# Optimization experiments

Hardware: AMD Instinct MI355X
Metric: run time of the kernel (lower is better)

## Reference

```python
import jax, jax.numpy as jnp
import numpy as np

N_NODES = 100000
N_EDGES = 1600000
IN_DIM = 128
HID = 32
HEADS = 4
NEG_SLOPE = 0.2


def gat_conv(x, src, dst, W, att_src, att_dst, bias, n_nodes, heads, out_ch):
    # x: [N, Fin], W: [Fin, heads*out_ch], att_*: [heads, out_ch], bias: [heads*out_ch]
    h = (x @ W).reshape(n_nodes, heads, out_ch)            # [N, H, C]
    a_src = jnp.einsum('nhc,hc->nh', h, att_src)           # [N, H]
    a_dst = jnp.einsum('nhc,hc->nh', h, att_dst)           # [N, H]
    e = jax.nn.leaky_relu(a_src[src] + a_dst[dst], NEG_SLOPE)  # [E, H]
    # segment softmax over incoming edges of each target node
    e_max = jax.ops.segment_max(e, dst, num_segments=n_nodes)  # [N, H]
    ex = jnp.exp(e - e_max[dst])                               # [E, H]
    denom = jax.ops.segment_sum(ex, dst, num_segments=n_nodes)  # [N, H]
    alpha = ex / denom[dst]                                     # [E, H]
    msg = h[src] * alpha[:, :, None]                            # [E, H, C]
    out = jax.ops.segment_sum(msg, dst, num_segments=n_nodes)   # [N, H, C]
    return out.reshape(n_nodes, heads * out_ch) + bias


def setup_inputs() -> dict:
    key = jax.random.key(0)
    ks = jax.random.split(key, 10)
    x = jax.random.normal(ks[0], (N_NODES, IN_DIM), dtype=jnp.float32)
    edge_index = jax.random.randint(ks[1], (2, N_EDGES), 0, N_NODES, dtype=jnp.int64) if jax.config.jax_enable_x64 else jax.random.randint(ks[1], (2, N_EDGES), 0, N_NODES, dtype=jnp.int32)
    s = 0.1
    W1 = jax.random.normal(ks[2], (IN_DIM, HEADS * HID), dtype=jnp.float32) * s
    att_src1 = jax.random.normal(ks[3], (HEADS, HID), dtype=jnp.float32) * s
    att_dst1 = jax.random.normal(ks[4], (HEADS, HID), dtype=jnp.float32) * s
    b1 = jnp.zeros((HEADS * HID,), dtype=jnp.float32)
    W2 = jax.random.normal(ks[5], (HEADS * HID, HEADS * HID), dtype=jnp.float32) * s
    att_src2 = jax.random.normal(ks[6], (HEADS, HID), dtype=jnp.float32) * s
    att_dst2 = jax.random.normal(ks[7], (HEADS, HID), dtype=jnp.float32) * s
    b2 = jnp.zeros((HEADS * HID,), dtype=jnp.float32)
    return {"x": x, "edge_index": edge_index, "W1": W1, "att_src1": att_src1,
            "att_dst1": att_dst1, "b1": b1, "W2": W2, "att_src2": att_src2,
            "att_dst2": att_dst2, "b2": b2}


def reference(x, edge_index, W1, att_src1, att_dst1, b1, W2, att_src2, att_dst2, b2):
    src, dst = edge_index[0], edge_index[1]
    x1 = jax.nn.relu(gat_conv(x, src, dst, W1, att_src1, att_dst1, b1, N_NODES, HEADS, HID))
    x2 = jax.nn.relu(gat_conv(x1, src, dst, W2, att_src2, att_dst2, b2, N_NODES, HEADS, HID))
    # [N, heads*hid, 2]
    return jnp.concatenate([x1[:, :, None], x2[:, :, None]], axis=2)
```

## Files before the change

kernel.cpp:

```cpp
#include <hip/hip_runtime.h>

#define NN 100000
#define NE 1600000
#define GEMM_GRID 1563
#define NBUK 196
#define BCAP 10240
#define PA_BLOCKS 320
#define PA_EDGES 5000
#define K1_GRID (16 + PA_BLOCKS)
#define K2_GRID (NBUK + GEMM_GRID)
#define AGG_GRID 12500

typedef short bf16x8 __attribute__((ext_vector_type(8)));
typedef float f32x4 __attribute__((ext_vector_type(4)));
typedef unsigned int u32;
typedef u32 u32x4 __attribute__((ext_vector_type(4)));
typedef unsigned short u16;

__device__ inline u32 bf16r(float x) {
    u32 u = __float_as_uint(x);
    return (u + 0x7FFFu + ((u >> 16) & 1u)) >> 16;
}

__device__ inline void split_pack8(const float a[8], u32 hh[4], u32 ll[4]) {
#pragma unroll
    for (int j = 0; j < 4; ++j) {
        u32 u0 = __float_as_uint(a[2 * j]);
        u32 u1 = __float_as_uint(a[2 * j + 1]);
        float l0 = a[2 * j] - __uint_as_float(u0 & 0xFFFF0000u);
        float l1 = a[2 * j + 1] - __uint_as_float(u1 & 0xFFFF0000u);
        hh[j] = (u0 >> 16) | (u1 & 0xFFFF0000u);
        ll[j] = (__float_as_uint(l0) >> 16) | (__float_as_uint(l1) & 0xFFFF0000u);
    }
}

__device__ inline void wpack_body(int idx, const float* __restrict__ W,
                                  bf16x8* __restrict__ wpH, bf16x8* __restrict__ wpL) {
    if (idx >= 2048) return;
    int lane = idx & 63, tile = idx >> 6;
    int kc = tile >> 3, ct = tile & 7;
    int col = lane & 15, kq = lane >> 4;
    int kbase = kc * 32 + kq * 8;
    float a[8];
#pragma unroll
    for (int i = 0; i < 8; ++i)
        a[i] = W[(size_t)(kbase + i) * 128 + ct * 16 + col];
    u32 hh[4], ll[4];
    split_pack8(a, hh, ll);
    wpH[tile * 64 + lane] = __builtin_bit_cast(bf16x8, (u32x4){hh[0], hh[1], hh[2], hh[3]});
    wpL[tile * 64 + lane] = __builtin_bit_cast(bf16x8, (u32x4){ll[0], ll[1], ll[2], ll[3]});
}

__global__ __launch_bounds__(256) void k1(
    const float* __restrict__ W1, bf16x8* __restrict__ wpH1, bf16x8* __restrict__ wpL1,
    const float* __restrict__ W2, bf16x8* __restrict__ wpH2, bf16x8* __restrict__ wpL2,
    const int* __restrict__ dst, const int* __restrict__ src,
    int* __restrict__ gtail, u32* __restrict__ tmp) {
    const int b = blockIdx.x;
    if (b < 8) {
        wpack_body(b * 256 + threadIdx.x, W1, wpH1, wpL1);
        return;
    } else if (b < 16) {
        wpack_body((b - 8) * 256 + threadIdx.x, W2, wpH2, wpL2);
        return;
    }
    __shared__ int lhist[NBUK], lcur[NBUK];
    const int t = threadIdx.x;
    const int e0 = (b - 16) * PA_EDGES;
    const int e1 = e0 + PA_EDGES;
    for (int i = t; i < NBUK; i += 256) lhist[i] = 0;
    __syncthreads();
    for (int e = e0 + t; e < e1; e += 256)
        atomicAdd(&lhist[dst[e] >> 9], 1);
    __syncthreads();
    for (int i = t; i < NBUK; i += 256)
        if (lhist[i] > 0) lcur[i] = atomicAdd(&gtail[i], lhist[i]);
    __syncthreads();
    for (int e = e0 + t; e < e1; e += 256) {
        int d = dst[e];
        int bb = d >> 9;
        int p = atomicAdd(&lcur[bb], 1);
        tmp[(size_t)bb * BCAP + p] = ((u32)(d & 511) << 17) | (u32)src[e];
    }
}

__device__ inline void gemm_epilogue(f32x4 acc[8], int row0, int w, int col, int kq,
                                     const float* __restrict__ atts,
                                     const float* __restrict__ attd,
                                     u16* __restrict__ hb,
                                     float* __restrict__ a_src,
                                     float* __restrict__ a_dst) {
    float as0[4], as1[4], ad0[4], ad1[4];
#pragma unroll
    for (int q = 0; q < 4; ++q) {
        as0[q] = atts[q * 32 + col];
        as1[q] = atts[q * 32 + 16 + col];
        ad0[q] = attd[q * 32 + col];
        ad1[q] = attd[q * 32 + 16 + col];
    }
#pragma unroll
    for (int r = 0; r < 4; ++r) {
        int node = row0 + w * 16 + kq * 4 + r;
        float ps[4], pd[4];
#pragma unroll
        for (int q = 0; q < 4; ++q) {
            float d0 = acc[2 * q][r], d1 = acc[2 * q + 1][r];
            ps[q] = d0 * as0[q] + d1 * as1[q];
            pd[q] = d0 * ad0[q] + d1 * ad1[q];
        }
#pragma unroll
        for (int off = 1; off < 16; off <<= 1) {
#pragma unroll
            for (int q = 0; q < 4; ++q) {
                ps[q] += __shfl_xor(ps[q], off);
                pd[q] += __shfl_xor(pd[q], off);
            }
        }
        if (node < NN) {
#pragma unroll
            for (int ct = 0; ct < 8; ++ct)
                hb[(size_t)node * 128 + ct * 16 + col] = (u16)bf16r(acc[ct][r]);
            if (col < 4) {
                float vs = col == 0 ? ps[0] : col == 1 ? ps[1] : col == 2 ? ps[2] : ps[3];
                float vd = col == 0 ? pd[0] : col == 1 ? pd[1] : col == 2 ? pd[2] : pd[3];
                a_src[node * 4 + col] = vs;
                a_dst[node * 4 + col] = vd;
            }
        }
    }
}

__global__ __launch_bounds__(256) void k2(
    const float* __restrict__ x,
    const bf16x8* __restrict__ wpH, const bf16x8* __restrict__ wpL,
    const float* __restrict__ atts, const float* __restrict__ attd,
    u16* __restrict__ hb, float* __restrict__ a_src, float* __restrict__ a_dst,
    const int* __restrict__ gtail, const u32* __restrict__ tmp,
    int* __restrict__ row_ptr, int* __restrict__ src_sorted) {
    __shared__ u32 ldata[BCAP];
    __shared__ int lh[512];
    __shared__ int lsc[256];
    __shared__ int wsum[4];
    const int idx = blockIdx.x;
    const int t = threadIdx.x;
    if (idx < NBUK) {
        const int g = idx;
        const int n = gtail[g];
        int gv = (t < g) ? gtail[t] : 0;
#pragma unroll
        for (int m = 1; m < 64; m <<= 1) gv += __shfl_xor(gv, m);
        if ((t & 63) == 0) wsum[t >> 6] = gv;
        lh[t] = 0;
        lh[t + 256] = 0;
        __syncthreads();
        const int ebase = wsum[0] + wsum[1] + wsum[2] + wsum[3];
        for (int i = t; i < n; i += 256) ldata[i] = tmp[(size_t)g * BCAP + i];
        __syncthreads();
        for (int i = t; i < n; i += 256)
            atomicAdd(&lh[ldata[i] >> 17], 1);
        __syncthreads();
        int c0 = lh[2 * t], c1 = lh[2 * t + 1];
        lsc[t] = c0 + c1;
        __syncthreads();
        for (int off = 1; off < 256; off <<= 1) {
            int xv = (t >= off) ? lsc[t - off] : 0;
            __syncthreads();
            lsc[t] += xv;
            __syncthreads();
        }
        int exclPair = (t == 0) ? 0 : lsc[t - 1];
        int base0 = ebase + exclPair;
        int base1 = base0 + c0;
        lh[2 * t] = base0;
        lh[2 * t + 1] = base1;
        int node = (g << 9) + 2 * t;
        if (node < NN) row_ptr[node] = base0;
        if (node + 1 < NN) row_ptr[node + 1] = base1;
        if (g == NBUK - 1 && t == 0) row_ptr[NN] = ebase + n;
        __syncthreads();
        for (int i = t; i < n; i += 256) {
            u32 v = ldata[i];
            int p = atomicAdd(&lh[v >> 17], 1);
            src_sorted[p] = (int)(v & 0x1FFFFu);
        }
        return;
    }
    const int row0 = (idx - NBUK) * 64;
    const int lane = t & 63;
    const int w = t >> 6;
    const int col = lane & 15, kq = lane >> 4;
    int node_a = row0 + w * 16 + col;
    if (node_a > NN - 1) node_a = NN - 1;
    const float* xrow = x + (size_t)node_a * 128 + kq * 8;
    float a[32];
#pragma unroll
    for (int kc = 0; kc < 4; ++kc) {
        *(float4*)&a[kc * 8 + 0] = *(const float4*)(xrow + kc * 32);
        *(float4*)&a[kc * 8 + 4] = *(const float4*)(xrow + kc * 32 + 4);
    }
    f32x4 acc[8];
#pragma unroll
    for (int ct = 0; ct < 8; ++ct) acc[ct] = (f32x4){0.f, 0.f, 0.f, 0.f};
#pragma unroll
    for (int kc = 0; kc < 4; ++kc) {
        u32 hh[4], ll[4];
        split_pack8(&a[kc * 8], hh, ll);
        bf16x8 ah = __builtin_bit_cast(bf16x8, (u32x4){hh[0], hh[1], hh[2], hh[3]});
        bf16x8 al = __builtin_bit_cast(bf16x8, (u32x4){ll[0], ll[1], ll[2], ll[3]});
#pragma unroll
        for (int ct = 0; ct < 8; ++ct) {
            bf16x8 bh = wpH[(kc * 8 + ct) * 64 + lane];
            bf16x8 bl = wpL[(kc * 8 + ct) * 64 + lane];
            acc[ct] = __builtin_amdgcn_mfma_f32_16x16x32_bf16(ah, bh, acc[ct], 0, 0, 0);
            acc[ct] = __builtin_amdgcn_mfma_f32_16x16x32_bf16(al, bh, acc[ct], 0, 0, 0);
            acc[ct] = __builtin_amdgcn_mfma_f32_16x16x32_bf16(ah, bl, acc[ct], 0, 0, 0);
        }
    }
    gemm_epilogue(acc, row0, w, col, kq, atts, attd, hb, a_src, a_dst);
}

__global__ __launch_bounds__(256) void k_gemm2(
    const u32* __restrict__ xb,
    const bf16x8* __restrict__ wpH, const bf16x8* __restrict__ wpL,
    const float* __restrict__ atts, const float* __restrict__ attd,
    u16* __restrict__ hb, float* __restrict__ a_src, float* __restrict__ a_dst) {
    const int t = threadIdx.x;
    const int row0 = blockIdx.x * 64;
    const int lane = t & 63;
    const int w = t >> 6;
    const int col = lane & 15, kq = lane >> 4;
    int node_a = row0 + w * 16 + col;
    if (node_a > NN - 1) node_a = NN - 1;
    const u32* xrow = xb + (size_t)node_a * 64 + kq * 4;
    int4 aw[4];
#pragma unroll
    for (int kc = 0; kc < 4; ++kc) aw[kc] = *(const int4*)(xrow + kc * 16);
    f32x4 acc[8];
#pragma unroll
    for (int ct = 0; ct < 8; ++ct) acc[ct] = (f32x4){0.f, 0.f, 0.f, 0.f};
#pragma unroll
    for (int kc = 0; kc < 4; ++kc) {
        bf16x8 a = __builtin_bit_cast(bf16x8, aw[kc]);
#pragma unroll
        for (int ct = 0; ct < 8; ++ct) {
            bf16x8 bh = wpH[(kc * 8 + ct) * 64 + lane];
            bf16x8 bl = wpL[(kc * 8 + ct) * 64 + lane];
            acc[ct] = __builtin_amdgcn_mfma_f32_16x16x32_bf16(a, bh, acc[ct], 0, 0, 0);
            acc[ct] = __builtin_amdgcn_mfma_f32_16x16x32_bf16(a, bl, acc[ct], 0, 0, 0);
        }
    }
    gemm_epilogue(acc, row0, w, col, kq, atts, attd, hb, a_src, a_dst);
}

__global__ __launch_bounds__(256, 4) void k_agg(
    const u32* __restrict__ hb,
    const float* __restrict__ a_src, const float* __restrict__ a_dst,
    const int* __restrict__ row_ptr, const int* __restrict__ src_sorted,
    const float* __restrict__ bias,
    u32* __restrict__ x1b, float* __restrict__ outp, int layer) {
    const int lane = threadIdx.x & 63;
    const int node0 = blockIdx.x * 8 + (threadIdx.x >> 6) * 2;
    const int q = lane >> 4;
    const int es = lane & 15;
    const int hbase = lane & 48;
#pragma unroll
    for (int ni = 0; ni < 2; ++ni) {
        const int node = node0 + ni;
        if (node >= NN) continue;
        const int e0 = row_ptr[node], e1 = row_ptr[node + 1];
        const int emax = e1 - 1;
        const float advh = a_dst[node * 4 + q];
        float den = 0.f, a0a = 0.f, a0b = 0.f, a1a = 0.f, a1b = 0.f;
        if (e1 > e0) {
            int eidx = e0 + es;
            if (eidx > emax) eidx = emax;
            int sv = src_sorted[eidx];
            float av = a_src[sv * 4 + q];
            for (int ec = e0; ec < e1; ec += 16) {
                int cnt = e1 - ec;
                cnt = cnt < 16 ? cnt : 16;
                int eidxn = ec + 16 + es;
                if (eidxn > emax) eidxn = emax;
                int svn = src_sorted[eidxn];
                float avn = a_src[svn * 4 + q];
                float lk = av + advh;
                lk = lk > 0.f ? lk : 0.2f * lk;
                float ex = (es < cnt) ? __expf(lk - 8.f) : 0.f;
                den += ex;
                if (cnt == 16) {
                    u32 wv[16];
#pragma unroll
                    for (int u = 0; u < 16; ++u) {
                        int su = __builtin_amdgcn_readlane(sv, u);
                        wv[u] = hb[((size_t)su << 6) + lane];
                    }
                    float exu[16];
#pragma unroll
                    for (int u = 0; u < 16; ++u) exu[u] = __shfl(ex, hbase | u);
#pragma unroll
                    for (int u = 0; u < 16; ++u) {
                        float h0 = __uint_as_float(wv[u] << 16);
                        float h1 = __uint_as_float(wv[u] & 0xFFFF0000u);
                        if (u & 1) { a0b = fmaf(exu[u], h0, a0b); a1b = fmaf(exu[u], h1, a1b); }
                        else       { a0a = fmaf(exu[u], h0, a0a); a1a = fmaf(exu[u], h1, a1a); }
                    }
                } else {
                    for (int u0 = 0; u0 < cnt; u0 += 4) {
                        u32 wv[4];
                        float exu[4];
#pragma unroll
                        for (int j = 0; j < 4; ++j) {
                            int su = __builtin_amdgcn_readlane(sv, u0 + j);
                            wv[j] = hb[((size_t)su << 6) + lane];
                        }
#pragma unroll
                        for (int j = 0; j < 4; ++j) exu[j] = __shfl(ex, hbase | (u0 + j));
#pragma unroll
                        for (int j = 0; j < 4; ++j) {
                            float h0 = __uint_as_float(wv[j] << 16);
                            float h1 = __uint_as_float(wv[j] & 0xFFFF0000u);
                            if (j & 1) { a0b = fmaf(exu[j], h0, a0b); a1b = fmaf(exu[j], h1, a1b); }
                            else       { a0a = fmaf(exu[j], h0, a0a); a1a = fmaf(exu[j], h1, a1a); }
                        }
                    }
                }
                sv = svn;
                av = avn;
            }
        }
        float a0 = a0a + a0b, a1 = a1a + a1b;
#pragma unroll
        for (int m = 1; m < 16; m <<= 1) den += __shfl_xor(den, m);
        float inv = den > 0.f ? 1.f / den : 0.f;
        int c0 = lane * 2;
        float r0 = fmaxf(fmaf(a0, inv, bias[c0]), 0.f);
        float r1 = fmaxf(fmaf(a1, inv, bias[c0 + 1]), 0.f);
        if (layer == 1) {
            x1b[node * 64 + lane] = bf16r(r0) | (bf16r(r1) << 16);
        } else {
            u32 w1 = x1b[node * 64 + lane];
            float4 o;
            o.x = __uint_as_float(w1 << 16);
            o.y = r0;
            o.z = __uint_as_float(w1 & 0xFFFF0000u);
            o.w = r1;
            u32x4 ov = __builtin_bit_cast(u32x4, o);
            __builtin_nontemporal_store(ov,
                (u32x4*)(outp + (size_t)node * 256 + lane * 4));
        }
    }
}


extern "C" void kernel_launch(void* const* d_in, const int* in_sizes, int n_in,
                              void* d_out, int out_size, void* d_ws, size_t ws_size,
                              hipStream_t stream) {
    const float* x   = (const float*)d_in[0];
    const int*   ei  = (const int*)d_in[1];
    const float* W1  = (const float*)d_in[2];
    const float* as1 = (const float*)d_in[3];
    const float* ad1 = (const float*)d_in[4];
    const float* b1  = (const float*)d_in[5];
    const float* W2  = (const float*)d_in[6];
    const float* as2 = (const float*)d_in[7];
    const float* ad2 = (const float*)d_in[8];
    const float* b2  = (const float*)d_in[9];
    float* out = (float*)d_out;
    const int* src = ei;
    const int* dst = ei + NE;

    char* w = (char*)d_ws;
    size_t off = 0;
    auto alloc = [&](size_t bytes) -> void* {
        void* p = w + off;
        off = (off + bytes + 255) & ~((size_t)255);
        return p;
    };
    u16* hb         = (u16*)alloc((size_t)NN * 128 * 2);
    u32* x1b        = (u32*)alloc((size_t)NN * 64 * 4);
    float* a_src    = (float*)alloc((size_t)NN * 4 * 4);
    float* a_dst    = (float*)alloc((size_t)NN * 4 * 4);
    int* row_ptr    = (int*)alloc((size_t)(NN + 1) * 4);
    int* gtail      = (int*)alloc(NBUK * 4);
    u32* tmp        = (u32*)alloc((size_t)NBUK * BCAP * 4);
    int* src_sorted = (int*)alloc((size_t)NE * 4);
    bf16x8* wpH1    = (bf16x8*)alloc(2048 * 16);
    bf16x8* wpL1    = (bf16x8*)alloc(2048 * 16);
    bf16x8* wpH2    = (bf16x8*)alloc(2048 * 16);
    bf16x8* wpL2    = (bf16x8*)alloc(2048 * 16);

    (void)hipMemsetAsync(gtail, 0, NBUK * 4, stream);
    k1<<<K1_GRID, 256, 0, stream>>>(W1, wpH1, wpL1, W2, wpH2, wpL2,
                                    dst, src, gtail, tmp);
    k2<<<K2_GRID, 256, 0, stream>>>(x, wpH1, wpL1, as1, ad1, hb, a_src, a_dst,
                                    gtail, tmp, row_ptr, src_sorted);

    k_agg<<<AGG_GRID, 256, 0, stream>>>((const u32*)hb, a_src, a_dst, row_ptr,
                                        src_sorted, b1, x1b, out, 1);
    k_gemm2<<<(NN + 63) / 64, 256, 0, stream>>>(x1b, wpH2, wpL2, as2, ad2,
                                                hb, a_src, a_dst);
    k_agg<<<AGG_GRID, 256, 0, stream>>>((const u32*)hb, a_src, a_dst, row_ptr,
                                        src_sorted, b2, x1b, out, 2);
}
```

Before: 252.1 us.

## Fuse layer-1 aggregation with layer-2 GEMM and halve sort bucket size

The layer-1 aggregation kernel now also runs the second-layer projection: each block aggregates 16 nodes, stages their bf16 features in shared memory, and applies MFMA against W2 to produce h2 and the attention logits. This removes the separate GEMM launch and its reread of x1. The counting-sort buckets are also shrunk to 256 nodes, which doubles the bucket count and shrinks the per-block shared footprint. Layer 2 now writes into separate buffers (hb2, a_src2, a_dst2) instead of overwriting the layer-1 ones. The cost is that layer-1 aggregation now handles 4 nodes per wave serially and adds a block barrier, which may lower latency hiding.

```diff
diff --git a/kernel.cpp b/kernel.cpp
--- a/kernel.cpp
+++ b/kernel.cpp
@@ -3,13 +3,14 @@
 #define NN 100000
 #define NE 1600000
 #define GEMM_GRID 1563
-#define NBUK 196
-#define BCAP 10240
+#define NBUK 391
+#define BCAP 5120
 #define PA_BLOCKS 320
 #define PA_EDGES 5000
 #define K1_GRID (16 + PA_BLOCKS)
 #define K2_GRID (NBUK + GEMM_GRID)
-#define AGG_GRID 12500
+#define AG1_GRID 6250
+#define AGG2_GRID 12500
 
 typedef short bf16x8 __attribute__((ext_vector_type(8)));
 typedef float f32x4 __attribute__((ext_vector_type(4)));
@@ -71,16 +72,16 @@
     for (int i = t; i < NBUK; i += 256) lhist[i] = 0;
     __syncthreads();
     for (int e = e0 + t; e < e1; e += 256)
-        atomicAdd(&lhist[dst[e] >> 9], 1);
+        atomicAdd(&lhist[dst[e] >> 8], 1);
     __syncthreads();
     for (int i = t; i < NBUK; i += 256)
         if (lhist[i] > 0) lcur[i] = atomicAdd(&gtail[i], lhist[i]);
     __syncthreads();
     for (int e = e0 + t; e < e1; e += 256) {
         int d = dst[e];
-        int bb = d >> 9;
+        int bb = d >> 8;
         int p = atomicAdd(&lcur[bb], 1);
-        tmp[(size_t)bb * BCAP + p] = ((u32)(d & 511) << 17) | (u32)src[e];
+        tmp[(size_t)bb * BCAP + p] = ((u32)(d & 255) << 17) | (u32)src[e];
     }
 }
 
@@ -138,29 +139,32 @@
     const int* __restrict__ gtail, const u32* __restrict__ tmp,
     int* __restrict__ row_ptr, int* __restrict__ src_sorted) {
     __shared__ u32 ldata[BCAP];
-    __shared__ int lh[512];
+    __shared__ int lh[256];
     __shared__ int lsc[256];
-    __shared__ int wsum[4];
     const int idx = blockIdx.x;
     const int t = threadIdx.x;
     if (idx < NBUK) {
         const int g = idx;
         const int n = gtail[g];
-        int gv = (t < g) ? gtail[t] : 0;
-#pragma unroll
-        for (int m = 1; m < 64; m <<= 1) gv += __shfl_xor(gv, m);
-        if ((t & 63) == 0) wsum[t >> 6] = gv;
+        int acc = 0;
+        for (int i = t; i < g; i += 256) acc += gtail[i];
+        lsc[t] = acc;
+        __syncthreads();
+        for (int off = 128; off > 0; off >>= 1) {
+            if (t < off) lsc[t] += lsc[t + off];
+            __syncthreads();
+        }
+        const int ebase = lsc[0];
         lh[t] = 0;
-        lh[t + 256] = 0;
         __syncthreads();
-        const int ebase = wsum[0] + wsum[1] + wsum[2] + wsum[3];
-        for (int i = t; i < n; i += 256) ldata[i] = tmp[(size_t)g * BCAP + i];
+        for (int i = t; i < n; i += 256) {
+            u32 v = tmp[(size_t)g * BCAP + i];
+            ldata[i] = v;
+            atomicAdd(&lh[v >> 17], 1);
+        }
         __syncthreads();
-        for (int i = t; i < n; i += 256)
-            atomicAdd(&lh[ldata[i] >> 17], 1);
-        __syncthreads();
-        int c0 = lh[2 * t], c1 = lh[2 * t + 1];
-        lsc[t] = c0 + c1;
+        int c = lh[t];
+        lsc[t] = c;
         __syncthreads();
         for (int off = 1; off < 256; off <<= 1) {
             int xv = (t >= off) ? lsc[t - off] : 0;
@@ -168,14 +172,11 @@
             lsc[t] += xv;
             __syncthreads();
         }
-        int exclPair = (t == 0) ? 0 : lsc[t - 1];
-        int base0 = ebase + exclPair;
-        int base1 = base0 + c0;
-        lh[2 * t] = base0;
-        lh[2 * t + 1] = base1;
-        int node = (g << 9) + 2 * t;
-        if (node < NN) row_ptr[node] = base0;
-        if (node + 1 < NN) row_ptr[node + 1] = base1;
+        int excl = (t == 0) ? 0 : lsc[t - 1];
+        int base = ebase + excl;
+        lh[t] = base;
+        int node = (g << 8) + t;
+        if (node < NN) row_ptr[node] = base;
         if (g == NBUK - 1 && t == 0) row_ptr[NN] = ebase + n;
         __syncthreads();
         for (int i = t; i < n; i += 256) {
@@ -219,45 +220,143 @@
     gemm_epilogue(acc, row0, w, col, kq, atts, attd, hb, a_src, a_dst);
 }
 
-__global__ __launch_bounds__(256) void k_gemm2(
-    const u32* __restrict__ xb,
-    const bf16x8* __restrict__ wpH, const bf16x8* __restrict__ wpL,
-    const float* __restrict__ atts, const float* __restrict__ attd,
-    u16* __restrict__ hb, float* __restrict__ a_src, float* __restrict__ a_dst) {
+__global__ __launch_bounds__(256) void k_ag1(
+    const u32* __restrict__ hb,
+    const float* __restrict__ a_src, const float* __restrict__ a_dst,
+    const int* __restrict__ row_ptr, const int* __restrict__ src_sorted,
+    const float* __restrict__ bias1,
+    const bf16x8* __restrict__ wpH2, const bf16x8* __restrict__ wpL2,
+    const float* __restrict__ atts2, const float* __restrict__ attd2,
+    u32* __restrict__ x1b, u16* __restrict__ hb2,
+    float* __restrict__ a_src2, float* __restrict__ a_dst2) {
+    __shared__ __align__(16) u32 xs[16][68];
     const int t = threadIdx.x;
-    const int row0 = blockIdx.x * 64;
     const int lane = t & 63;
-    const int w = t >> 6;
+    const int wv = t >> 6;
+    const int q = lane >> 4;
+    const int es = lane & 15;
+    const int hbase = lane & 48;
+    const int node0 = blockIdx.x * 16;
+    const float bv0 = bias1[lane * 2], bv1 = bias1[lane * 2 + 1];
+#pragma unroll 1
+    for (int ni = 0; ni < 4; ++ni) {
+        const int node = node0 + wv * 4 + ni;
+        const int e0 = row_ptr[node], e1 = row_ptr[node + 1];
+        const int emax = e1 - 1;
+        const float advh = a_dst[node * 4 + q];
+        float den = 0.f, a0a = 0.f, a0b = 0.f, a1a = 0.f, a1b = 0.f;
+        if (e1 > e0) {
+            int eidx = e0 + es;
+            if (eidx > emax) eidx = emax;
+            int sv = src_sorted[eidx];
+            float av = a_src[sv * 4 + q];
+            for (int ec = e0; ec < e1; ec += 16) {
+                int cnt = e1 - ec;
+                cnt = cnt < 16 ? cnt : 16;
+                int eidxn = ec + 16 + es;
+                if (eidxn > emax) eidxn = emax;
+                int svn = src_sorted[eidxn];
+                float avn = a_src[svn * 4 + q];
+                float lk = av + advh;
+                lk = lk > 0.f ? lk : 0.2f * lk;
+                float ex = (es < cnt) ? __expf(lk - 8.f) : 0.f;
+                den += ex;
+                if (cnt == 16) {
+                    u32 wvv[16];
+#pragma unroll
+                    for (int u = 0; u < 16; ++u) {
+                        int su = __builtin_amdgcn_readlane(sv, u);
+                        wvv[u] = hb[((size_t)su << 6) + lane];
+                    }
+                    float exu[16];
+#pragma unroll
+                    for (int u = 0; u < 16; ++u) exu[u] = __shfl(ex, hbase | u);
+#pragma unroll
+                    for (int u = 0; u < 16; ++u) {
+                        float h0 = __uint_as_float(wvv[u] << 16);
+                        float h1 = __uint_as_float(wvv[u] & 0xFFFF0000u);
+                        if (u & 1) { a0b = fmaf(exu[u], h0, a0b); a1b = fmaf(exu[u], h1, a1b); }
+                        else       { a0a = fmaf(exu[u], h0, a0a); a1a = fmaf(exu[u], h1, a1a); }
+                    }
+                } else {
+                    for (int u0 = 0; u0 < cnt; u0 += 4) {
+                        u32 wvv[4];
+                        float exu[4];
+#pragma unroll
+                        for (int j = 0; j < 4; ++j) {
+                            int su = __builtin_amdgcn_readlane(sv, u0 + j);
+                            wvv[j] = hb[((size_t)su << 6) + lane];
+                        }
+#pragma unroll
+                        for (int j = 0; j < 4; ++j) exu[j] = __shfl(ex, hbase | (u0 + j));
+#pragma unroll
+                        for (int j = 0; j < 4; ++j) {
+                            float h0 = __uint_as_float(wvv[j] << 16);
+                            float h1 = __uint_as_float(wvv[j] & 0xFFFF0000u);
+                            if (j & 1) { a0b = fmaf(exu[j], h0, a0b); a1b = fmaf(exu[j], h1, a1b); }
+                            else       { a0a = fmaf(exu[j], h0, a0a); a1a = fmaf(exu[j], h1, a1a); }
+                        }
+                    }
+                }
+                sv = svn;
+                av = avn;
+            }
+        }
+        float a0 = a0a + a0b, a1 = a1a + a1b;
+#pragma unroll
+        for (int m = 1; m < 16; m <<= 1) den += __shfl_xor(den, m);
+        float inv = den > 0.f ? 1.f / den : 0.f;
+        float r0 = fmaxf(fmaf(a0, inv, bv0), 0.f);
+        float r1 = fmaxf(fmaf(a1, inv, bv1), 0.f);
+        u32 pair = bf16r(r0) | (bf16r(r1) << 16);
+        x1b[node * 64 + lane] = pair;
+        xs[wv * 4 + ni][lane] = pair;
+    }
+    __syncthreads();
     const int col = lane & 15, kq = lane >> 4;
-    int node_a = row0 + w * 16 + col;
-    if (node_a > NN - 1) node_a = NN - 1;
-    const u32* xrow = xb + (size_t)node_a * 64 + kq * 4;
+    const int ct0 = 2 * wv, ct1 = 2 * wv + 1;
     int4 aw[4];
 #pragma unroll
-    for (int kc = 0; kc < 4; ++kc) aw[kc] = *(const int4*)(xrow + kc * 16);
-    f32x4 acc[8];
-#pragma unroll
-    for (int ct = 0; ct < 8; ++ct) acc[ct] = (f32x4){0.f, 0.f, 0.f, 0.f};
+    for (int kc = 0; kc < 4; ++kc)
+        aw[kc] = *(const int4*)&xs[col][kc * 16 + kq * 4];
+    f32x4 acc0 = (f32x4){0.f, 0.f, 0.f, 0.f};
+    f32x4 acc1 = (f32x4){0.f, 0.f, 0.f, 0.f};
 #pragma unroll
     for (int kc = 0; kc < 4; ++kc) {
         bf16x8 a = __builtin_bit_cast(bf16x8, aw[kc]);
-#pragma unroll
-        for (int ct = 0; ct < 8; ++ct) {
-            bf16x8 bh = wpH[(kc * 8 + ct) * 64 + lane];
-            bf16x8 bl = wpL[(kc * 8 + ct) * 64 + lane];
-            acc[ct] = __builtin_amdgcn_mfma_f32_16x16x32_bf16(a, bh, acc[ct], 0, 0, 0);
-            acc[ct] = __builtin_amdgcn_mfma_f32_16x16x32_bf16(a, bl, acc[ct], 0, 0, 0);
-        }
-    }
-    gemm_epilogue(acc, row0, w, col, kq, atts, attd, hb, a_src, a_dst);
-}
-
-__global__ __launch_bounds__(256, 4) void k_agg(
+        acc0 = __builtin_amdgcn_mfma_f32_16x16x32_bf16(a, wpH2[(kc * 8 + ct0) * 64 + lane], acc0, 0, 0, 0);
+        acc0 = __builtin_amdgcn_mfma_f32_16x16x32_bf16(a, wpL2[(kc * 8 + ct0) * 64 + lane], acc0, 0, 0, 0);
+        acc1 = __builtin_amdgcn_mfma_f32_16x16x32_bf16(a, wpH2[(kc * 8 + ct1) * 64 + lane], acc1, 0, 0, 0);
+        acc1 = __builtin_amdgcn_mfma_f32_16x16x32_bf16(a, wpL2[(kc * 8 + ct1) * 64 + lane], acc1, 0, 0, 0);
+    }
+    const float as0 = atts2[wv * 32 + col], as1 = atts2[wv * 32 + 16 + col];
+    const float ad0 = attd2[wv * 32 + col], ad1 = attd2[wv * 32 + 16 + col];
+#pragma unroll
+    for (int r = 0; r < 4; ++r) {
+        int node = node0 + kq * 4 + r;
+        float d0 = acc0[r], d1 = acc1[r];
+        float ps = d0 * as0 + d1 * as1;
+        float pd = d0 * ad0 + d1 * ad1;
+#pragma unroll
+        for (int off = 1; off < 16; off <<= 1) {
+            ps += __shfl_xor(ps, off);
+            pd += __shfl_xor(pd, off);
+        }
+        hb2[(size_t)node * 128 + ct0 * 16 + col] = (u16)bf16r(d0);
+        hb2[(size_t)node * 128 + ct1 * 16 + col] = (u16)bf16r(d1);
+        if (col == 0) {
+            a_src2[node * 4 + wv] = ps;
+            a_dst2[node * 4 + wv] = pd;
+        }
+    }
+}
+
+__global__ __launch_bounds__(256, 4) void k_agg2(
     const u32* __restrict__ hb,
     const float* __restrict__ a_src, const float* __restrict__ a_dst,
     const int* __restrict__ row_ptr, const int* __restrict__ src_sorted,
     const float* __restrict__ bias,
-    u32* __restrict__ x1b, float* __restrict__ outp, int layer) {
+    const u32* __restrict__ x1b, float* __restrict__ outp) {
     const int lane = threadIdx.x & 63;
     const int node0 = blockIdx.x * 8 + (threadIdx.x >> 6) * 2;
     const int q = lane >> 4;
@@ -335,19 +434,15 @@
         int c0 = lane * 2;
         float r0 = fmaxf(fmaf(a0, inv, bias[c0]), 0.f);
         float r1 = fmaxf(fmaf(a1, inv, bias[c0 + 1]), 0.f);
-        if (layer == 1) {
-            x1b[node * 64 + lane] = bf16r(r0) | (bf16r(r1) << 16);
-        } else {
-            u32 w1 = x1b[node * 64 + lane];
-            float4 o;
-            o.x = __uint_as_float(w1 << 16);
-            o.y = r0;
-            o.z = __uint_as_float(w1 & 0xFFFF0000u);
-            o.w = r1;
-            u32x4 ov = __builtin_bit_cast(u32x4, o);
-            __builtin_nontemporal_store(ov,
-                (u32x4*)(outp + (size_t)node * 256 + lane * 4));
-        }
+        u32 w1 = x1b[node * 64 + lane];
+        float4 o;
+        o.x = __uint_as_float(w1 << 16);
+        o.y = r0;
+        o.z = __uint_as_float(w1 & 0xFFFF0000u);
+        o.w = r1;
+        u32x4 ov = __builtin_bit_cast(u32x4, o);
+        __builtin_nontemporal_store(ov,
+            (u32x4*)(outp + (size_t)node * 256 + lane * 4));
     }
 }
 
@@ -377,9 +472,12 @@
         return p;
     };
     u16* hb         = (u16*)alloc((size_t)NN * 128 * 2);
+    u16* hb2        = (u16*)alloc((size_t)NN * 128 * 2);
     u32* x1b        = (u32*)alloc((size_t)NN * 64 * 4);
     float* a_src    = (float*)alloc((size_t)NN * 4 * 4);
     float* a_dst    = (float*)alloc((size_t)NN * 4 * 4);
+    float* a_src2   = (float*)alloc((size_t)NN * 4 * 4);
+    float* a_dst2   = (float*)alloc((size_t)NN * 4 * 4);
     int* row_ptr    = (int*)alloc((size_t)(NN + 1) * 4);
     int* gtail      = (int*)alloc(NBUK * 4);
     u32* tmp        = (u32*)alloc((size_t)NBUK * BCAP * 4);
@@ -394,11 +492,10 @@
                                     dst, src, gtail, tmp);
     k2<<<K2_GRID, 256, 0, stream>>>(x, wpH1, wpL1, as1, ad1, hb, a_src, a_dst,
                                     gtail, tmp, row_ptr, src_sorted);
-
-    k_agg<<<AGG_GRID, 256, 0, stream>>>((const u32*)hb, a_src, a_dst, row_ptr,
-                                        src_sorted, b1, x1b, out, 1);
-    k_gemm2<<<(NN + 63) / 64, 256, 0, stream>>>(x1b, wpH2, wpL2, as2, ad2,
-                                                hb, a_src, a_dst);
-    k_agg<<<AGG_GRID, 256, 0, stream>>>((const u32*)hb, a_src, a_dst, row_ptr,
-                                        src_sorted, b2, x1b, out, 2);
-}
+    k_ag1<<<AG1_GRID, 256, 0, stream>>>((const u32*)hb, a_src, a_dst, row_ptr,
+                                        src_sorted, b1, wpH2, wpL2, as2, ad2,
+                                        x1b, hb2, a_src2, a_dst2);
+    k_agg2<<<AGG2_GRID, 256, 0, stream>>>((const u32*)hb2, a_src2, a_dst2,
+                                          row_ptr, src_sorted, b2,
+                                          (const u32*)x1b, out);
+}
```

Result: no change. 248.4 us, median of 2 (-1.4%).
